# Optimization experiments

Measured on AMD Instinct MI355X. Metric: run time of the kernel, lower is better.

The kernel has to match this reference:

```python
import jax, jax.numpy as jnp
import numpy as np

HIDDEN_SIZE = 16
INPUT_SIZE = 32
BATCH = 4096
SEQ = 512


def setup_inputs() -> dict:
    key = jax.random.key(0)
    ks = jax.random.split(key, 7)
    H, I = HIDDEN_SIZE, INPUT_SIZE
    s_ih = 1.0 / np.sqrt(H)
    inp = {
        "x": jax.random.normal(ks[0], (BATCH, SEQ, I), dtype=jnp.float32),
        # PyTorch LSTM params, gate order (i, f, g, o), uniform(-1/sqrt(H), 1/sqrt(H))
        "W_ih": jax.random.uniform(ks[1], (4 * H, I), minval=-s_ih, maxval=s_ih, dtype=jnp.float32),
        "W_hh": jax.random.uniform(ks[2], (4 * H, H), minval=-s_ih, maxval=s_ih, dtype=jnp.float32),
        "b_ih": jax.random.uniform(ks[3], (4 * H,), minval=-s_ih, maxval=s_ih, dtype=jnp.float32),
        "b_hh": jax.random.uniform(ks[4], (4 * H,), minval=-s_ih, maxval=s_ih, dtype=jnp.float32),
        "fc_w": jax.random.uniform(ks[5], (1, H), minval=-s_ih, maxval=s_ih, dtype=jnp.float32),
        "fc_b": jax.random.uniform(ks[6], (1,), minval=-s_ih, maxval=s_ih, dtype=jnp.float32),
    }
    return inp


def reference(x, W_ih, W_hh, b_ih, b_hh, fc_w, fc_b):
    B, T, I = x.shape
    H = HIDDEN_SIZE
    # Precompute input contribution to all gates for all timesteps: [B, T, 4H]
    xg = jnp.einsum("bti,gi->btg", x, W_ih) + (b_ih + b_hh)

    def step(carry, xg_t):
        h, c = carry  # each [B, H]
        gates = xg_t + h @ W_hh.T  # [B, 4H]
        i_g, f_g, g_g, o_g = jnp.split(gates, 4, axis=-1)
        i_g = jax.nn.sigmoid(i_g)
        f_g = jax.nn.sigmoid(f_g)
        g_g = jnp.tanh(g_g)
        o_g = jax.nn.sigmoid(o_g)
        c_new = f_g * c + i_g * g_g
        h_new = o_g * jnp.tanh(c_new)
        return (h_new, c_new), None

    h0 = jnp.zeros((B, H), dtype=x.dtype)
    c0 = jnp.zeros((B, H), dtype=x.dtype)
    (h_last, _), _ = jax.lax.scan(step, (h0, c0), jnp.swapaxes(xg, 0, 1))
    # dropout is identity in eval mode; take last-step hidden -> fc -> sigmoid
    return jax.nn.sigmoid(h_last @ fc_w.T + fc_b)  # [B, 1]
```

## Files before the change

### kernel.cpp

```cpp
#include <hip/hip_runtime.h>


constexpr int BATCH = 4096;
constexpr int SEQ   = 512;
constexpr int ISZ   = 32;
constexpr int HSZ   = 16;
constexpr int CH    = 32;
constexpr int NCH   = SEQ / CH;
constexpr int XGS   = 66;

typedef __fp16 h2  __attribute__((ext_vector_type(2)));
typedef __fp16 v8h __attribute__((ext_vector_type(8)));
typedef float  v4f __attribute__((ext_vector_type(4)));

union H8 { v8h v; h2 h[4]; };

__device__ __forceinline__ float swz_xor16(float v) {
  return __int_as_float(__builtin_amdgcn_ds_swizzle(__float_as_int(v), 0x401F));
}
__device__ __forceinline__ float swz_xor1(float v) {
  return __int_as_float(__builtin_amdgcn_ds_swizzle(__float_as_int(v), 0x041F));
}
__device__ __forceinline__ float rcpf_(float x) { return __builtin_amdgcn_rcpf(x); }
__device__ __forceinline__ float rl_f(float v, int l) {
  return __int_as_float(__builtin_amdgcn_readlane(__float_as_int(v), l));
}

__global__ __launch_bounds__(256, 4) void lstm_fused(
    const float* __restrict__ x, const float* __restrict__ Wih,
    const float* __restrict__ Whh, const float* __restrict__ bih,
    const float* __restrict__ bhh, const float* __restrict__ fcw,
    const float* __restrict__ fcb, float* __restrict__ out) {
  const int lane = threadIdx.x & 63;
  const int wid  = __builtin_amdgcn_readfirstlane(threadIdx.x >> 6);
  const int bidx = blockIdx.x * 4 + wid;
  const int col  = lane & 15;
  const int kg   = lane >> 4;
  const bool q1  = (kg == 1);
  const bool q3  = (kg == 3);
  const bool isg = (kg == 2);
  const float sS = isg ? -2.f : -1.f;
  const float sA = isg ?  2.f :  1.f;
  const float sB = isg ? -1.f :  0.f;

  __shared__ float xg_s[4][CH * XGS];

  H8 bfr[4];
  float bb[4];
#pragma unroll
  for (int nt = 0; nt < 4; ++nt) {
    const int g = nt * 16 + col;
    const float* wp = Wih + g * ISZ + kg * 8;
    const v4f w0 = *reinterpret_cast<const v4f*>(wp);
    const v4f w1 = *reinterpret_cast<const v4f*>(wp + 4);
    bfr[nt].h[0] = __builtin_amdgcn_cvt_pkrtz(w0.x, w0.y);
    bfr[nt].h[1] = __builtin_amdgcn_cvt_pkrtz(w0.z, w0.w);
    bfr[nt].h[2] = __builtin_amdgcn_cvt_pkrtz(w1.x, w1.y);
    bfr[nt].h[3] = __builtin_amdgcn_cvt_pkrtz(w1.z, w1.w);
    bb[nt] = bih[g] + bhh[g];
  }

  int whh[8];
  {
    const float* wp = Whh + lane * HSZ;
#pragma unroll
    for (int j = 0; j < 4; ++j) {
      const v4f v = *reinterpret_cast<const v4f*>(wp + 4 * j);
      whh[2 * j]     = __builtin_bit_cast(int, __builtin_amdgcn_cvt_pkrtz(v.x, v.y));
      whh[2 * j + 1] = __builtin_bit_cast(int, __builtin_amdgcn_cvt_pkrtz(v.z, v.w));
    }
  }

  const float* xb_ = x + (size_t)bidx * (SEQ * ISZ);
  const int aoff0 = col * ISZ + kg * 8;
  const int aoff1 = (16 + col) * ISZ + kg * 8;

  v4f pf[4];
  pf[0] = *reinterpret_cast<const v4f*>(xb_ + aoff0);
  pf[1] = *reinterpret_cast<const v4f*>(xb_ + aoff0 + 4);
  pf[2] = *reinterpret_cast<const v4f*>(xb_ + aoff1);
  pf[3] = *reinterpret_cast<const v4f*>(xb_ + aoff1 + 4);

  float* wbase = &xg_s[wid][(kg * 4) * XGS + col];
  const float* xrd = &xg_s[wid][lane];

  int hs_pk[8];
#pragma unroll
  for (int j = 0; j < 8; ++j) hs_pk[j] = 0;
  float c = 0.f, hlast = 0.f;

  for (int ch = 0; ch < NCH; ++ch) {
    H8 afr0, afr1;
    afr0.h[0] = __builtin_amdgcn_cvt_pkrtz(pf[0].x, pf[0].y);
    afr0.h[1] = __builtin_amdgcn_cvt_pkrtz(pf[0].z, pf[0].w);
    afr0.h[2] = __builtin_amdgcn_cvt_pkrtz(pf[1].x, pf[1].y);
    afr0.h[3] = __builtin_amdgcn_cvt_pkrtz(pf[1].z, pf[1].w);
    afr1.h[0] = __builtin_amdgcn_cvt_pkrtz(pf[2].x, pf[2].y);
    afr1.h[1] = __builtin_amdgcn_cvt_pkrtz(pf[2].z, pf[2].w);
    afr1.h[2] = __builtin_amdgcn_cvt_pkrtz(pf[3].x, pf[3].y);
    afr1.h[3] = __builtin_amdgcn_cvt_pkrtz(pf[3].z, pf[3].w);

    {
      const int nc = (ch + 1 < NCH) ? (ch + 1) : 0;
      const float* nx = xb_ + (size_t)nc * (CH * ISZ);
      pf[0] = *reinterpret_cast<const v4f*>(nx + aoff0);
      pf[1] = *reinterpret_cast<const v4f*>(nx + aoff0 + 4);
      pf[2] = *reinterpret_cast<const v4f*>(nx + aoff1);
      pf[3] = *reinterpret_cast<const v4f*>(nx + aoff1 + 4);
    }
    __builtin_amdgcn_sched_barrier(0);

#pragma unroll
    for (int nt = 0; nt < 4; ++nt) {
      const v4f ci = {bb[nt], bb[nt], bb[nt], bb[nt]};
      const v4f d0 = __builtin_amdgcn_mfma_f32_16x16x32_f16(afr0.v, bfr[nt].v, ci, 0, 0, 0);
      const v4f d1 = __builtin_amdgcn_mfma_f32_16x16x32_f16(afr1.v, bfr[nt].v, ci, 0, 0, 0);
#pragma unroll
      for (int r = 0; r < 4; ++r) {
        wbase[r * XGS + nt * 16]        = d0[r];
        wbase[(16 + r) * XGS + nt * 16] = d1[r];
      }
    }

    float xcur = xrd[0];
#pragma unroll
    for (int s = 0; s < CH; ++s) {
      const float xnxt = xrd[(s + 1 < CH) ? (s + 1) * XGS : 0];
      float a0 = xcur, a1 = 0.f;
#pragma unroll
      for (int j = 0; j < 4; ++j) {
        a0 = __builtin_amdgcn_fdot2(__builtin_bit_cast(h2, whh[j]),
                                    __builtin_bit_cast(h2, hs_pk[j]), a0, false);
        a1 = __builtin_amdgcn_fdot2(__builtin_bit_cast(h2, whh[j + 4]),
                                    __builtin_bit_cast(h2, hs_pk[j + 4]), a1, false);
      }
      const float pre = a0 + a1;
      const float e_ = __expf(pre * sS);
      const float y  = fmaf(sA, rcpf_(1.f + e_), sB);
      int va = __float_as_int(y), vb = va;
      asm volatile("s_nop 0\n\tv_permlane32_swap_b32 %0, %1\n\ts_nop 0"
                   : "+v"(va), "+v"(vb));
      const float prt = __int_as_float(va ^ vb ^ __float_as_int(y));
      const float p1  = y * prt;
      const float p1x = swz_xor16(p1);
      const float sf  = q3 ? prt : y;
      c = fmaf(sf, c, p1x);
      const float e2 = __expf(-2.f * c);
      const float th = fmaf(2.f, rcpf_(1.f + e2), -1.f);
      const float so = q1 ? prt : y;
      hlast = so * th;
      const float hx = swz_xor1(hlast);
      const int hpi = __builtin_bit_cast(int, __builtin_amdgcn_cvt_pkrtz(hlast, hx));
#pragma unroll
      for (int j = 0; j < 8; ++j)
        hs_pk[j] = __builtin_amdgcn_readlane(hpi, 16 + 2 * j);
      xcur = xnxt;
    }
  }

  float s = fcb[0];
#pragma unroll
  for (int k = 0; k < HSZ; ++k) s = fmaf(rl_f(hlast, 16 + k), fcw[k], s);
  if (lane == 0) out[bidx] = rcpf_(1.f + __expf(-s));
}

extern "C" void kernel_launch(void* const* d_in, const int* in_sizes, int n_in,
                              void* d_out, int out_size, void* d_ws, size_t ws_size,
                              hipStream_t stream) {
  const float* x   = (const float*)d_in[0];
  const float* Wih = (const float*)d_in[1];
  const float* Whh = (const float*)d_in[2];
  const float* bih = (const float*)d_in[3];
  const float* bhh = (const float*)d_in[4];
  const float* fcw = (const float*)d_in[5];
  const float* fcb = (const float*)d_in[6];
  float* out = (float*)d_out;

  dim3 grid(BATCH / 4);
  dim3 block(256);
  hipLaunchKernelGGL(lstm_fused, grid, block, 0, stream,
                     x, Wih, Whh, bih, bhh, fcw, fcb, out);
}
```

Baseline: 458.2 us.

## Fold log2e into LSTM weights, shorten recurrent step dependency chain

Pre-scales the input and recurrent weights and biases by log2(e), doubled for the g gate, so each step's sigmoid and tanh use a raw exp2 with no extra multiply. Splits the 8-term fdot2 accumulation into four parallel chains to cut serial latency. Replaces ds_swizzle cross-lane moves with permlane16_swap and a DPP quad permute to avoid LDS-path latency, and prefetches xg two steps ahead. Rounding the scaled weights to fp16 adds a small change in numerical error.

```diff
diff --git a/kernel.cpp b/kernel.cpp
--- a/kernel.cpp
+++ b/kernel.cpp
@@ -9,21 +9,22 @@
 constexpr int NCH   = SEQ / CH;
 constexpr int XGS   = 66;
 
+constexpr float L2E = 1.44269504088896340736f;
+
 typedef __fp16 h2  __attribute__((ext_vector_type(2)));
 typedef __fp16 v8h __attribute__((ext_vector_type(8)));
 typedef float  v4f __attribute__((ext_vector_type(4)));
 
 union H8 { v8h v; h2 h[4]; };
 
-__device__ __forceinline__ float swz_xor16(float v) {
-  return __int_as_float(__builtin_amdgcn_ds_swizzle(__float_as_int(v), 0x401F));
-}
-__device__ __forceinline__ float swz_xor1(float v) {
-  return __int_as_float(__builtin_amdgcn_ds_swizzle(__float_as_int(v), 0x041F));
-}
 __device__ __forceinline__ float rcpf_(float x) { return __builtin_amdgcn_rcpf(x); }
+__device__ __forceinline__ float exp2f_(float x) { return __builtin_amdgcn_exp2f(x); }
 __device__ __forceinline__ float rl_f(float v, int l) {
   return __int_as_float(__builtin_amdgcn_readlane(__float_as_int(v), l));
+}
+__device__ __forceinline__ float dpp_xor1(float v) {
+  return __int_as_float(__builtin_amdgcn_update_dpp(
+      __float_as_int(v), __float_as_int(v), 0xB1, 0xF, 0xF, true));
 }
 
 __global__ __launch_bounds__(256, 4) void lstm_fused(
@@ -39,9 +40,9 @@
   const bool q1  = (kg == 1);
   const bool q3  = (kg == 3);
   const bool isg = (kg == 2);
-  const float sS = isg ? -2.f : -1.f;
   const float sA = isg ?  2.f :  1.f;
   const float sB = isg ? -1.f :  0.f;
+  const float M2 = -2.f * L2E;
 
   __shared__ float xg_s[4][CH * XGS];
 
@@ -50,24 +51,26 @@
 #pragma unroll
   for (int nt = 0; nt < 4; ++nt) {
     const int g = nt * 16 + col;
+    const float sc = (nt == 2) ? 2.f * L2E : L2E;
     const float* wp = Wih + g * ISZ + kg * 8;
     const v4f w0 = *reinterpret_cast<const v4f*>(wp);
     const v4f w1 = *reinterpret_cast<const v4f*>(wp + 4);
-    bfr[nt].h[0] = __builtin_amdgcn_cvt_pkrtz(w0.x, w0.y);
-    bfr[nt].h[1] = __builtin_amdgcn_cvt_pkrtz(w0.z, w0.w);
-    bfr[nt].h[2] = __builtin_amdgcn_cvt_pkrtz(w1.x, w1.y);
-    bfr[nt].h[3] = __builtin_amdgcn_cvt_pkrtz(w1.z, w1.w);
-    bb[nt] = bih[g] + bhh[g];
+    bfr[nt].h[0] = __builtin_amdgcn_cvt_pkrtz(w0.x * sc, w0.y * sc);
+    bfr[nt].h[1] = __builtin_amdgcn_cvt_pkrtz(w0.z * sc, w0.w * sc);
+    bfr[nt].h[2] = __builtin_amdgcn_cvt_pkrtz(w1.x * sc, w1.y * sc);
+    bfr[nt].h[3] = __builtin_amdgcn_cvt_pkrtz(w1.z * sc, w1.w * sc);
+    bb[nt] = (bih[g] + bhh[g]) * sc;
   }
 
   int whh[8];
   {
+    const float wsc = isg ? 2.f * L2E : L2E;
     const float* wp = Whh + lane * HSZ;
 #pragma unroll
     for (int j = 0; j < 4; ++j) {
       const v4f v = *reinterpret_cast<const v4f*>(wp + 4 * j);
-      whh[2 * j]     = __builtin_bit_cast(int, __builtin_amdgcn_cvt_pkrtz(v.x, v.y));
-      whh[2 * j + 1] = __builtin_bit_cast(int, __builtin_amdgcn_cvt_pkrtz(v.z, v.w));
+      whh[2 * j]     = __builtin_bit_cast(int, __builtin_amdgcn_cvt_pkrtz(v.x * wsc, v.y * wsc));
+      whh[2 * j + 1] = __builtin_bit_cast(int, __builtin_amdgcn_cvt_pkrtz(v.z * wsc, v.w * wsc));
     }
   }
 
@@ -122,46 +125,58 @@
       }
     }
 
-    float xcur = xrd[0];
+    float xA = xrd[0];
+    float xB = xrd[XGS];
 #pragma unroll
     for (int s = 0; s < CH; ++s) {
-      const float xnxt = xrd[(s + 1 < CH) ? (s + 1) * XGS : 0];
-      float a0 = xcur, a1 = 0.f;
-#pragma unroll
-      for (int j = 0; j < 4; ++j) {
-        a0 = __builtin_amdgcn_fdot2(__builtin_bit_cast(h2, whh[j]),
-                                    __builtin_bit_cast(h2, hs_pk[j]), a0, false);
-        a1 = __builtin_amdgcn_fdot2(__builtin_bit_cast(h2, whh[j + 4]),
-                                    __builtin_bit_cast(h2, hs_pk[j + 4]), a1, false);
-      }
-      const float pre = a0 + a1;
-      const float e_ = __expf(pre * sS);
+      const float xC = xrd[(s + 2 < CH) ? (s + 2) * XGS : 0];
+      float t0 = __builtin_amdgcn_fdot2(__builtin_bit_cast(h2, whh[0]),
+                                        __builtin_bit_cast(h2, hs_pk[0]), xA, false);
+      float t1 = __builtin_amdgcn_fdot2(__builtin_bit_cast(h2, whh[2]),
+                                        __builtin_bit_cast(h2, hs_pk[2]), 0.f, false);
+      float t2 = __builtin_amdgcn_fdot2(__builtin_bit_cast(h2, whh[4]),
+                                        __builtin_bit_cast(h2, hs_pk[4]), 0.f, false);
+      float t3 = __builtin_amdgcn_fdot2(__builtin_bit_cast(h2, whh[6]),
+                                        __builtin_bit_cast(h2, hs_pk[6]), 0.f, false);
+      t0 = __builtin_amdgcn_fdot2(__builtin_bit_cast(h2, whh[1]),
+                                  __builtin_bit_cast(h2, hs_pk[1]), t0, false);
+      t1 = __builtin_amdgcn_fdot2(__builtin_bit_cast(h2, whh[3]),
+                                  __builtin_bit_cast(h2, hs_pk[3]), t1, false);
+      t2 = __builtin_amdgcn_fdot2(__builtin_bit_cast(h2, whh[5]),
+                                  __builtin_bit_cast(h2, hs_pk[5]), t2, false);
+      t3 = __builtin_amdgcn_fdot2(__builtin_bit_cast(h2, whh[7]),
+                                  __builtin_bit_cast(h2, hs_pk[7]), t3, false);
+      const float pre = (t0 + t1) + (t2 + t3);
+      const float e_ = exp2f_(-pre);
       const float y  = fmaf(sA, rcpf_(1.f + e_), sB);
       int va = __float_as_int(y), vb = va;
       asm volatile("s_nop 0\n\tv_permlane32_swap_b32 %0, %1\n\ts_nop 0"
                    : "+v"(va), "+v"(vb));
       const float prt = __int_as_float(va ^ vb ^ __float_as_int(y));
-      const float p1  = y * prt;
-      const float p1x = swz_xor16(p1);
+      const float p1 = y * prt;
+      int wa = __float_as_int(p1), wb = wa;
+      asm volatile("s_nop 0\n\tv_permlane16_swap_b32 %0, %1\n\ts_nop 0"
+                   : "+v"(wa), "+v"(wb));
+      const float p1x = __int_as_float(wa ^ wb ^ __float_as_int(p1));
       const float sf  = q3 ? prt : y;
       c = fmaf(sf, c, p1x);
-      const float e2 = __expf(-2.f * c);
+      const float e2 = exp2f_(c * M2);
       const float th = fmaf(2.f, rcpf_(1.f + e2), -1.f);
       const float so = q1 ? prt : y;
       hlast = so * th;
-      const float hx = swz_xor1(hlast);
+      const float hx = dpp_xor1(hlast);
       const int hpi = __builtin_bit_cast(int, __builtin_amdgcn_cvt_pkrtz(hlast, hx));
 #pragma unroll
       for (int j = 0; j < 8; ++j)
         hs_pk[j] = __builtin_amdgcn_readlane(hpi, 16 + 2 * j);
-      xcur = xnxt;
+      xA = xB; xB = xC;
     }
   }
 
   float s = fcb[0];
 #pragma unroll
   for (int k = 0; k < HSZ; ++k) s = fmaf(rl_f(hlast, 16 + k), fcw[k], s);
-  if (lane == 0) out[bidx] = rcpf_(1.f + __expf(-s));
+  if (lane == 0) out[bidx] = rcpf_(1.f + exp2f_(-s * L2E));
 }
 
 extern "C" void kernel_launch(void* const* d_in, const int* in_sizes, int n_in,
```

New measurement: 468.4 us. 2.2% more time.
